# Optimization experiments

Measured on AMD Instinct MI355X. Metric: run time of the kernel, lower is better.

Reference implementation:

```python
import jax, jax.numpy as jnp
import numpy as np

B, L, D = 2, 2048, 2048
N, K, H = 16, 8, 128
EPS = 1e-6
ROPE_THETA = 1000000
K_MASK = -2.3819763e+38


def rms_norm(x, w, eps=EPS):
    dtype = x.dtype
    rms = jnp.sqrt(jnp.mean(x.astype(jnp.float32) ** 2, axis=-1, keepdims=True) + eps)
    return (w * x / rms).astype(dtype)


def apply_rope(inputs, positions, head_dim, rope_theta=ROPE_THETA):
    # inputs: [B, L, n, H], positions: [B, L]
    fraction = 2 * jnp.arange(0, head_dim // 2, dtype=jnp.float32) / head_dim
    timescale = rope_theta ** fraction  # [H/2]
    sinusoid = positions[..., jnp.newaxis] / timescale[jnp.newaxis, jnp.newaxis, :]  # [B,L,H/2]
    sinusoid = sinusoid[..., jnp.newaxis, :]  # [B,L,1,H/2]
    sin, cos = jnp.sin(sinusoid), jnp.cos(sinusoid)
    first, second = jnp.split(inputs, 2, axis=-1)
    out = jnp.concatenate([first * cos - second * sin, second * cos + first * sin], axis=-1)
    return out.astype(inputs.dtype)


def setup_inputs() -> dict:
    key = jax.random.key(0)
    ks = jax.random.split(key, 6)
    x = jax.random.normal(ks[0], (B, L, D), dtype=jnp.float32)
    position_ids = jnp.broadcast_to(jnp.arange(L, dtype=jnp.int32)[None, :], (B, L))
    # causal mask [B, L, S]
    attn_mask = jnp.broadcast_to(jnp.tril(jnp.ones((L, L), dtype=bool))[None], (B, L, L))
    wq = jax.random.normal(ks[1], (D, N, H), dtype=jnp.float32) * 0.02
    wk = jax.random.normal(ks[2], (D, K, H), dtype=jnp.float32) * 0.02
    wv = jax.random.normal(ks[3], (D, K, H), dtype=jnp.float32) * 0.02
    wo = jax.random.normal(ks[4], (N, H, D), dtype=jnp.float32) * 0.02
    q_norm_w = jnp.ones((H,), dtype=jnp.float32)
    k_norm_w = jnp.ones((H,), dtype=jnp.float32)
    return {"x": x, "position_ids": position_ids, "attn_mask": attn_mask,
            "wq": wq, "wk": wk, "wv": wv, "wo": wo,
            "q_norm_w": q_norm_w, "k_norm_w": k_norm_w}


def reference(x, position_ids, attn_mask, wq, wk, wv, wo, q_norm_w, k_norm_w):
    scale = H ** (-0.5)
    q = jnp.einsum('BLD,DNH->BLNH', x, wq)  # [B,L,N,H]
    k = jnp.einsum('BSD,DKH->BSKH', x, wk)  # [B,S,K,H]
    v = jnp.einsum('BSD,DKH->BSKH', x, wv)
    q = rms_norm(q, q_norm_w)
    k = rms_norm(k, k_norm_w)
    q = apply_rope(q, position_ids, H)
    k = apply_rope(k, position_ids, H)
    b, l, n, h = q.shape
    s = k.shape[1]
    kk = k.shape[2]
    q = q.reshape((b, l, kk, n // kk, h))
    attn = jnp.einsum('BLKGH,BSKH->BKGLS', q, k) * scale
    attn = attn.reshape((b, n, l, s))
    attn = jnp.where(jnp.expand_dims(attn_mask, -3), attn, K_MASK)
    attn = jax.nn.softmax(attn.astype(jnp.float32), axis=-1).astype(k.dtype)
    attn = attn.reshape((b, kk, n // kk, l, s))
    qkv = jnp.einsum('BKGLS,BSKH->BLKGH', attn, v).reshape((b, l, n, h))
    out = jnp.einsum('BLNH,NHD->BLD', qkv, wo)
    return out
```

## Files before the change

### kernel.cpp

```cpp
#include <hip/hip_runtime.h>

#define B_ 2
#define L_ 2048
#define D_ 2048
#define NH_ 16
#define KH_ 8
#define HD_ 128

typedef __attribute__((ext_vector_type(8))) short short8;
typedef __attribute__((ext_vector_type(4))) short short4v;
typedef __attribute__((ext_vector_type(4))) float floatx4;

__device__ __forceinline__ unsigned short f2bf(float f) {
  unsigned u = __float_as_uint(f);
  unsigned r = (u + 0x7fffu + ((u >> 16) & 1u)) >> 16;
  return (unsigned short)r;
}
__device__ __forceinline__ float bf2f(unsigned short h) {
  return __uint_as_float(((unsigned)h) << 16);
}
__device__ __forceinline__ void gl_lds16(const void* g, void* l) {
  __builtin_amdgcn_global_load_lds(
      (const __attribute__((address_space(1))) unsigned int*)g,
      (__attribute__((address_space(3))) unsigned int*)l, 16, 0, 0);
}
__device__ __forceinline__ void barrier_lds_only() {
  asm volatile("s_waitcnt lgkmcnt(0)" ::: "memory");
  __builtin_amdgcn_s_barrier();
}

__global__ __launch_bounds__(256) void prep1(const float* __restrict__ x,
                                             const float* __restrict__ wq,
                                             const float* __restrict__ wk,
                                             const float* __restrict__ wv,
                                             const float* __restrict__ wo,
                                             unsigned short* __restrict__ xb,
                                             unsigned short* __restrict__ wqkv_t,
                                             unsigned short* __restrict__ wo_t) {
  int id = blockIdx.x;
  int t = threadIdx.x;
  if (id < 8192) {
    long i = ((long)id * 256 + t) * 4;
    float4 v = *(const float4*)(x + i);
    ushort4 o;
    o.x = f2bf(v.x); o.y = f2bf(v.y); o.z = f2bf(v.z); o.w = f2bf(v.w);
    *(ushort4*)(xb + i) = o;
    return;
  }
  id -= 8192;
  __shared__ float tile[32][33];
  const float* in;
  unsigned short* out;
  int C, sh;
  if (id < 4096) {
    in = wq; out = wqkv_t; C = 2048; sh = 6;
  } else if (id < 6144) {
    in = wk; out = wqkv_t + 2048L * 2048; C = 1024; sh = 5; id -= 4096;
  } else if (id < 8192) {
    in = wv; out = wqkv_t + 3072L * 2048; C = 1024; sh = 5; id -= 6144;
  } else {
    in = wo; out = wo_t; C = 2048; sh = 6; id -= 8192;
  }
  int c0 = (id & ((1 << sh) - 1)) * 32, r0 = (id >> sh) * 32;
  int tx = t & 31, ty = t >> 5;
#pragma unroll
  for (int i = 0; i < 4; i++)
    tile[ty + i * 8][tx] = in[(long)(r0 + ty + i * 8) * C + c0 + tx];
  __syncthreads();
#pragma unroll
  for (int i = 0; i < 4; i++) {
    int oc = ty + i * 8;
    out[(long)(c0 + oc) * 2048 + r0 + tx] = f2bf(tile[tx][oc]);
  }
}

__global__ __launch_bounds__(256) void prep2(const unsigned short* __restrict__ qkv,
                                             const int* __restrict__ pos,
                                             const float* __restrict__ qw,
                                             const float* __restrict__ kw,
                                             unsigned short* __restrict__ qo,
                                             unsigned short* __restrict__ ko,
                                             unsigned short* __restrict__ vT) {
  int id = blockIdx.x;
  int t = threadIdx.x;
  if (id < 24576) {
    const int lane = t & 63, w = t >> 6;
    const int gid = id * 4 + w;
    const int row = gid / 24;
    const int hd = gid - row * 24;
    const int b = row >> 11, l = row & 2047;
    const unsigned short* src = qkv + (long)row * 4096 + hd * 128;
    float x0 = bf2f(src[lane]);
    float x1 = bf2f(src[lane + 64]);
    float ss = x0 * x0 + x1 * x1;
#pragma unroll
    for (int off = 32; off; off >>= 1) ss += __shfl_xor(ss, off);
    float inv = 1.0f / sqrtf(ss * (1.0f / 128.0f) + 1e-6f);
    const float* nw = (hd < 16) ? qw : kw;
    x0 = nw[lane] * x0 * inv;
    x1 = nw[lane + 64] * x1 * inv;
    float p = (float)pos[row];
    float ang = p * exp2f((float)lane * -0.31143075889f);
    float s, c;
    sincosf(ang, &s, &c);
    float o0 = x0 * c - x1 * s;
    float o1 = x1 * c + x0 * s;
    unsigned short* dst;
    if (hd < 16) {
      const float QSC = 0.08838834764831845f * 1.4426950408889634f;
      o0 *= QSC;
      o1 *= QSC;
      dst = qo + (((long)b * NH_ + hd) * L_ + l) * HD_;
    } else {
      dst = ko + (((long)b * KH_ + (hd - 16)) * L_ + l) * HD_;
    }
    dst[lane] = f2bf(o0);
    dst[lane + 64] = f2bf(o1);
    return;
  }
  id -= 24576;
  __shared__ unsigned short tile[32][33];
  int l0 = (id & 63) * 32, h0 = ((id >> 6) & 3) * 32;
  int bk = id >> 8;
  int b = bk >> 3, kh = bk & 7;
  int tx = t & 31, ty = t >> 5;
  const unsigned short* src = qkv + (long)b * L_ * 4096 + 3072 + kh * 128;
#pragma unroll
  for (int i = 0; i < 4; i++)
    tile[ty + i * 8][tx] = src[(long)(l0 + ty + i * 8) * 4096 + h0 + tx];
  __syncthreads();
  unsigned short* dst = vT + (long)bk * HD_ * L_;
#pragma unroll
  for (int i = 0; i < 4; i++)
    dst[(long)(h0 + ty + i * 8) * L_ + l0 + tx] = tile[tx][ty + i * 8];
}

template <int MODE>
__global__ __launch_bounds__(256, 3) void gemm128(const unsigned short* __restrict__ A,
                                                  const unsigned short* __restrict__ Bt,
                                                  void* __restrict__ C,
                                                  int M, int N, int K) {
  __shared__ unsigned short As[128 * 64];
  __shared__ unsigned short Bs[128 * 64];
  const int t = threadIdx.x;
  const int lane = t & 63, w = t >> 6;
  const int wy = w >> 1, wx = w & 1;
  const int col = lane & 15, quad = lane >> 4;
  const long m0 = (long)blockIdx.y * 128, n0 = (long)blockIdx.x * 128;
  floatx4 acc[4][4];
#pragma unroll
  for (int i = 0; i < 4; i++)
#pragma unroll
    for (int j = 0; j < 4; j++) acc[i][j] = (floatx4)0.0f;
  const int rs = t >> 3, bs = t & 7;
  for (int kt = 0; kt < K; kt += 64) {
#pragma unroll
    for (int i = 0; i < 4; i++) {
      int r = i * 32 + rs;
      gl_lds16(A + (m0 + r) * (long)K + kt + ((bs ^ (r & 7)) << 3),
               &As[(i * 32 + w * 8) * 64]);
      gl_lds16(Bt + (n0 + r) * (long)K + kt + ((bs ^ (r & 7)) << 3),
               &Bs[(i * 32 + w * 8) * 64]);
    }
    __syncthreads();
#pragma unroll
    for (int ks = 0; ks < 2; ks++) {
      short8 af[4], bf[4];
#pragma unroll
      for (int mi = 0; mi < 4; mi++) {
        int row = wy * 64 + mi * 16 + col;
        int blk = ks * 4 + quad;
        af[mi] = *(const short8*)&As[row * 64 + ((blk ^ (row & 7)) << 3)];
      }
#pragma unroll
      for (int ni = 0; ni < 4; ni++) {
        int row = wx * 64 + ni * 16 + col;
        int blk = ks * 4 + quad;
        bf[ni] = *(const short8*)&Bs[row * 64 + ((blk ^ (row & 7)) << 3)];
      }
#pragma unroll
      for (int mi = 0; mi < 4; mi++)
#pragma unroll
        for (int ni = 0; ni < 4; ni++)
          acc[mi][ni] = __builtin_amdgcn_mfma_f32_16x16x32_bf16(af[mi], bf[ni],
                                                                acc[mi][ni], 0, 0, 0);
    }
    __syncthreads();
  }
#pragma unroll
  for (int mi = 0; mi < 4; mi++)
#pragma unroll
    for (int r = 0; r < 4; r++) {
      long row = m0 + wy * 64 + mi * 16 + quad * 4 + r;
#pragma unroll
      for (int ni = 0; ni < 4; ni++) {
        long cg = n0 + wx * 64 + ni * 16 + col;
        float val = acc[mi][ni][r];
        if (MODE == 1)
          ((unsigned short*)C)[row * N + cg] = f2bf(val);
        else
          ((float*)C)[row * N + cg] = val;
      }
    }
}

template <int MODE>
__global__ __launch_bounds__(512, 2) void gemm256(const unsigned short* __restrict__ A,
                                                  const unsigned short* __restrict__ Bt,
                                                  void* __restrict__ C,
                                                  int M, int N, int K) {
  __shared__ unsigned short As[2][256 * 64];
  __shared__ unsigned short Bs[2][256 * 64];
  const int t = threadIdx.x;
  const int lane = t & 63, w = t >> 6;
  const int wy = w >> 2, wx = w & 3;
  const int col = lane & 15, quad = lane >> 4;
  const long m0 = (long)blockIdx.y * 256, n0 = (long)blockIdx.x * 256;
  const int rs = t >> 3, bs = t & 7;
  const int nt = K >> 6;

#define SA256(bufi, Tt, h)                                                      \
  gl_lds16(A + (m0 + (h) * 64 + rs) * (long)K + (long)(Tt) * 64 +               \
               ((bs ^ (rs & 7)) << 3),                                          \
           &As[bufi][((h) * 64 + w * 8) * 64])
#define SB256(bufi, Tt, h)                                                      \
  gl_lds16(Bt + (n0 + (h) * 64 + rs) * (long)K + (long)(Tt) * 64 +              \
                ((bs ^ (rs & 7)) << 3),                                         \
           &Bs[bufi][((h) * 64 + w * 8) * 64])

  floatx4 acc[8][4];
#pragma unroll
  for (int i = 0; i < 8; i++)
#pragma unroll
    for (int j = 0; j < 4; j++) acc[i][j] = (floatx4)0.0f;

  SA256(0, 0, 0); SA256(0, 0, 1); SA256(0, 0, 2); SA256(0, 0, 3);
  SB256(0, 0, 0); SB256(0, 0, 1); SB256(0, 0, 2); SB256(0, 0, 3);
  SB256(1, 1, 0); SB256(1, 1, 1); SB256(1, 1, 2); SB256(1, 1, 3);
  asm volatile("s_waitcnt vmcnt(4)" ::: "memory");
  __builtin_amdgcn_s_barrier();

  for (int T = 0; T < nt; ++T) {
    const int c = T & 1;
    const unsigned short* Ac = As[c];
    const unsigned short* Bc = Bs[c];
    short8 a[4][2], b[4][2];

#pragma unroll
    for (int mi = 0; mi < 4; mi++)
#pragma unroll
      for (int ks = 0; ks < 2; ks++) {
        int row = wy * 128 + mi * 16 + col;
        a[mi][ks] = *(const short8*)&Ac[row * 64 + (((ks * 4 + quad) ^ (row & 7)) << 3)];
      }
#pragma unroll
    for (int ni = 0; ni < 2; ni++)
#pragma unroll
      for (int ks = 0; ks < 2; ks++) {
        int row = wx * 64 + ni * 16 + col;
        b[ni][ks] = *(const short8*)&Bc[row * 64 + (((ks * 4 + quad) ^ (row & 7)) << 3)];
      }
    if (T + 1 < nt) { SA256(c ^ 1, T + 1, 0); SA256(c ^ 1, T + 1, 2); }
    __builtin_amdgcn_s_barrier();
    asm volatile("s_waitcnt lgkmcnt(0)" ::: "memory");
    __builtin_amdgcn_s_setprio(1);
#pragma unroll
    for (int mi = 0; mi < 4; mi++)
#pragma unroll
      for (int ni = 0; ni < 2; ni++)
#pragma unroll
        for (int ks = 0; ks < 2; ks++)
          acc[mi][ni] = __builtin_amdgcn_mfma_f32_16x16x32_bf16(a[mi][ks], b[ni][ks],
                                                                acc[mi][ni], 0, 0, 0);
    __builtin_amdgcn_s_setprio(0);
    __builtin_amdgcn_s_barrier();

#pragma unroll
    for (int ni = 2; ni < 4; ni++)
#pragma unroll
      for (int ks = 0; ks < 2; ks++) {
        int row = wx * 64 + ni * 16 + col;
        b[ni][ks] = *(const short8*)&Bc[row * 64 + (((ks * 4 + quad) ^ (row & 7)) << 3)];
      }
    if (T + 1 < nt) { SA256(c ^ 1, T + 1, 1); SA256(c ^ 1, T + 1, 3); }
    __builtin_amdgcn_s_barrier();
    asm volatile("s_waitcnt lgkmcnt(0)" ::: "memory");
    __builtin_amdgcn_s_setprio(1);
#pragma unroll
    for (int mi = 0; mi < 4; mi++)
#pragma unroll
      for (int ni = 2; ni < 4; ni++)
#pragma unroll
        for (int ks = 0; ks < 2; ks++)
          acc[mi][ni] = __builtin_amdgcn_mfma_f32_16x16x32_bf16(a[mi][ks], b[ni][ks],
                                                                acc[mi][ni], 0, 0, 0);
    __builtin_amdgcn_s_setprio(0);
    __builtin_amdgcn_s_barrier();

#pragma unroll
    for (int mi = 0; mi < 4; mi++)
#pragma unroll
      for (int ks = 0; ks < 2; ks++) {
        int row = wy * 128 + (mi + 4) * 16 + col;
        a[mi][ks] = *(const short8*)&Ac[row * 64 + (((ks * 4 + quad) ^ (row & 7)) << 3)];
      }
    if (T + 2 < nt) { SB256(c, T + 2, 0); SB256(c, T + 2, 1); }
    __builtin_amdgcn_s_barrier();
    asm volatile("s_waitcnt lgkmcnt(0)" ::: "memory");
    __builtin_amdgcn_s_setprio(1);
#pragma unroll
    for (int mi = 0; mi < 4; mi++)
#pragma unroll
      for (int ni = 0; ni < 2; ni++)
#pragma unroll
        for (int ks = 0; ks < 2; ks++)
          acc[mi + 4][ni] = __builtin_amdgcn_mfma_f32_16x16x32_bf16(a[mi][ks], b[ni][ks],
                                                                    acc[mi + 4][ni], 0, 0, 0);
    __builtin_amdgcn_s_setprio(0);
    __builtin_amdgcn_s_barrier();

    if (T + 2 < nt) { SB256(c, T + 2, 2); SB256(c, T + 2, 3); }
    __builtin_amdgcn_s_setprio(1);
#pragma unroll
    for (int mi = 0; mi < 4; mi++)
#pragma unroll
      for (int ni = 2; ni < 4; ni++)
#pragma unroll
        for (int ks = 0; ks < 2; ks++)
          acc[mi + 4][ni] = __builtin_amdgcn_mfma_f32_16x16x32_bf16(a[mi][ks], b[ni][ks],
                                                                    acc[mi + 4][ni], 0, 0, 0);
    __builtin_amdgcn_s_setprio(0);
    if (T + 1 < nt) {
      if (T >= nt - 2)
        asm volatile("s_waitcnt vmcnt(0)" ::: "memory");
      else
        asm volatile("s_waitcnt vmcnt(4)" ::: "memory");
      __builtin_amdgcn_s_barrier();
    }
  }
#undef SA256
#undef SB256

#pragma unroll
  for (int mi = 0; mi < 8; mi++)
#pragma unroll
    for (int r = 0; r < 4; r++) {
      long row = m0 + wy * 128 + mi * 16 + quad * 4 + r;
#pragma unroll
      for (int ni = 0; ni < 4; ni++) {
        long cg = n0 + wx * 64 + ni * 16 + col;
        float val = acc[mi][ni][r];
        if (MODE == 1)
          ((unsigned short*)C)[row * N + cg] = f2bf(val);
        else
          ((float*)C)[row * N + cg] = val;
      }
    }
}

__global__ __launch_bounds__(256, 2) void flash(const unsigned short* __restrict__ Q,
                                                const unsigned short* __restrict__ Kg,
                                                const unsigned short* __restrict__ VT,
                                                unsigned short* __restrict__ Og,
                                                float* __restrict__ Opart,
                                                float* __restrict__ lpart) {
  __shared__ unsigned short Ks[64 * 128];
  __shared__ unsigned short Vs[128 * 64];
  __shared__ unsigned short Ps[128 * 72];
  const int id = blockIdx.x;
  const int g = id & 255, r3 = id >> 8;
  const int kk3 = g & 7, nb = g >> 3;
  const int n = nb & 15, b = nb >> 4;
  int qt, st0, st1, chunk;
  if (r3 == 0) {
    qt = kk3; chunk = -1; st0 = 0; st1 = 2 * qt + 2;
  } else {
    qt = 15 - kk3;
    chunk = r3 - 1;
    const int half = qt + 1;
    st0 = chunk ? half : 0;
    st1 = chunk ? 2 * half : half;
  }
  const int steps_full = 2 * qt + 2;
  const int t = threadIdx.x, lane = t & 63, w = t >> 6;
  const int col = lane & 15, quad = lane >> 4;
  const int kvh = n >> 1;
  const unsigned short* kb = Kg + ((long)b * KH_ + kvh) * L_ * HD_;
  const unsigned short* vtb = VT + ((long)b * KH_ + kvh) * HD_ * L_;
  const int l0 = qt * 128;
  const unsigned short* qb = Q + (((long)b * NH_ + n) * L_ + l0) * HD_;

  const int rK = t >> 4, blkK = t & 15;
  const int rV = t >> 3, blkV = t & 7;

  short8 qf[2][4];
#pragma unroll
  for (int mi = 0; mi < 2; mi++)
#pragma unroll
    for (int ks = 0; ks < 4; ks++)
      qf[mi][ks] = *(const short8*)(qb + (w * 32 + mi * 16 + col) * 128 + ks * 32 + quad * 8);

  floatx4 o[2][8];
#pragma unroll
  for (int mi = 0; mi < 2; mi++)
#pragma unroll
    for (int nf = 0; nf < 8; nf++) o[mi][nf] = (floatx4)0.0f;
  float lrow[2] = {0.0f, 0.0f};

  {
    const long sb = (long)st0 * 64;
#pragma unroll
    for (int i = 0; i < 4; i++) {
      int r = i * 16 + rK;
      int gblk = (blkK & 8) | ((blkK ^ r) & 7);
      gl_lds16(kb + (sb + r) * 128 + gblk * 8, &Ks[(i * 16 + w * 4) * 128]);
    }
#pragma unroll
    for (int j = 0; j < 4; j++) {
      int r = j * 32 + rV;
      int gblk = (blkV ^ r) & 7;
      gl_lds16(vtb + (long)r * L_ + sb + gblk * 8, &Vs[(j * 32 + w * 8) * 64]);
    }
  }
  __syncthreads();

  short8 kpre[4], vpre[4];
  if (st0 + 1 < st1) {
    const long s0n = (long)(st0 + 1) * 64;
#pragma unroll
    for (int i = 0; i < 4; i++) {
      int r = i * 16 + rK;
      int gblk = (blkK & 8) | ((blkK ^ r) & 7);
      kpre[i] = *(const short8*)(kb + (s0n + r) * 128 + gblk * 8);
    }
#pragma unroll
    for (int j = 0; j < 4; j++) {
      int r = j * 32 + rV;
      int gblk = (blkV ^ r) & 7;
      vpre[j] = *(const short8*)(vtb + (long)r * L_ + s0n + gblk * 8);
    }
  }

  for (int st = st0; st < st1; st++) {
    const int s0 = st * 64;

    floatx4 sa[2][4];
#pragma unroll
    for (int mi = 0; mi < 2; mi++)
#pragma unroll
      for (int sf = 0; sf < 4; sf++) sa[mi][sf] = (floatx4)0.0f;
#pragma unroll
    for (int ks = 0; ks < 4; ks++) {
      short8 bf[4];
#pragma unroll
      for (int sf = 0; sf < 4; sf++) {
        int srow = sf * 16 + col;
        int blk = ks * 4 + quad;
        bf[sf] = *(const short8*)&Ks[srow * 128 + (((blk & 8) | ((blk ^ srow) & 7)) << 3)];
      }
#pragma unroll
      for (int mi = 0; mi < 2; mi++)
#pragma unroll
        for (int sf = 0; sf < 4; sf++)
          sa[mi][sf] = __builtin_amdgcn_mfma_f32_16x16x32_bf16(bf[sf], qf[mi][ks],
                                                               sa[mi][sf], 0, 0, 0);
    }

    if (st >= steps_full - 2) {
#pragma unroll
      for (int mi = 0; mi < 2; mi++) {
        int lg = l0 + w * 32 + mi * 16 + col;
#pragma unroll
        for (int sf = 0; sf < 4; sf++)
#pragma unroll
          for (int r = 0; r < 4; r++) {
            int sg = s0 + sf * 16 + quad * 4 + r;
            if (sg > lg) sa[mi][sf][r] = -3.0e38f;
          }
      }
    }

#pragma unroll
    for (int mi = 0; mi < 2; mi++)
#pragma unroll
      for (int sf = 0; sf < 4; sf++) {
        short4v pk;
#pragma unroll
        for (int r = 0; r < 4; r++) {
          float pv = exp2f(sa[mi][sf][r] - 17.0f);
          lrow[mi] += pv;
          pk[r] = (short)f2bf(pv);
        }
        *(short4v*)&Ps[(w * 32 + mi * 16 + col) * 72 + sf * 16 + quad * 4] = pk;
      }

#pragma unroll
    for (int ks = 0; ks < 2; ks++) {
      short8 pf[2];
#pragma unroll
      for (int mi = 0; mi < 2; mi++)
        pf[mi] = *(const short8*)&Ps[(w * 32 + mi * 16 + col) * 72 + ks * 32 + quad * 8];
      short8 vf[8];
#pragma unroll
      for (int nf = 0; nf < 8; nf++) {
        int h = nf * 16 + col;
        int blk = ks * 4 + quad;
        vf[nf] = *(const short8*)&Vs[h * 64 + ((blk ^ (h & 7)) << 3)];
      }
#pragma unroll
      for (int mi = 0; mi < 2; mi++)
#pragma unroll
        for (int nf = 0; nf < 8; nf++)
          o[mi][nf] = __builtin_amdgcn_mfma_f32_16x16x32_bf16(pf[mi], vf[nf],
                                                              o[mi][nf], 0, 0, 0);
    }

    barrier_lds_only();
    if (st + 1 < st1) {
#pragma unroll
      for (int i = 0; i < 4; i++) {
        int r = i * 16 + rK;
        *(short8*)&Ks[r * 128 + blkK * 8] = kpre[i];
      }
#pragma unroll
      for (int j = 0; j < 4; j++) {
        int r = j * 32 + rV;
        *(short8*)&Vs[r * 64 + blkV * 8] = vpre[j];
      }
      barrier_lds_only();
      if (st + 2 < st1) {
        const long s0n = (long)(st + 2) * 64;
#pragma unroll
        for (int i = 0; i < 4; i++) {
          int r = i * 16 + rK;
          int gblk = (blkK & 8) | ((blkK ^ r) & 7);
          kpre[i] = *(const short8*)(kb + (s0n + r) * 128 + gblk * 8);
        }
#pragma unroll
        for (int j = 0; j < 4; j++) {
          int r = j * 32 + rV;
          int gblk = (blkV ^ r) & 7;
          vpre[j] = *(const short8*)(vtb + (long)r * L_ + s0n + gblk * 8);
        }
      }
    }
  }

  if (chunk < 0) {
#pragma unroll
    for (int mi = 0; mi < 2; mi++) {
      float s = lrow[mi];
      s += __shfl_xor(s, 16);
      s += __shfl_xor(s, 32);
#pragma unroll
      for (int r = 0; r < 4; r++) {
        float inv = 1.0f / __shfl(s, quad * 4 + r);
        int lg = l0 + w * 32 + mi * 16 + quad * 4 + r;
        unsigned short* dst = Og + (((long)b * L_ + lg) * NH_ + n) * HD_;
#pragma unroll
        for (int nf = 0; nf < 8; nf++)
          dst[nf * 16 + col] = f2bf(o[mi][nf][r] * inv);
      }
    }
  } else {
    const int pidx = (((b * NH_ + n) * 8) + (qt - 8)) * 2 + chunk;
    float* Od = Opart + (long)pidx * 16384;
#pragma unroll
    for (int mi = 0; mi < 2; mi++) {
      float s = lrow[mi];
      s += __shfl_xor(s, 16);
      s += __shfl_xor(s, 32);
      if (lane < 16) lpart[pidx * 128 + w * 32 + mi * 16 + lane] = s;
#pragma unroll
      for (int r = 0; r < 4; r++) {
        int rl = w * 32 + mi * 16 + quad * 4 + r;
#pragma unroll
        for (int nf = 0; nf < 8; nf++)
          Od[rl * 128 + nf * 16 + col] = o[mi][nf][r];
      }
    }
  }
}

__global__ __launch_bounds__(256) void combine(const float* __restrict__ Opart,
                                               const float* __restrict__ lpart,
                                               unsigned short* __restrict__ Og) {
  const int id = blockIdx.x;
  const int q8 = id & 7, n = (id >> 3) & 15, b = id >> 7;
  const int pidx = (((b * NH_ + n) * 8) + q8) * 2;
  const float* OA = Opart + (long)pidx * 16384;
  const float* OB = OA + 16384;
  const int t = threadIdx.x;
  const int r = t >> 1, c0 = (t & 1) * 64;
  const float inv = 1.0f / (lpart[pidx * 128 + r] + lpart[(pidx + 1) * 128 + r]);
  const int lg = (8 + q8) * 128 + r;
  unsigned short* dst = Og + (((long)b * L_ + lg) * NH_ + n) * HD_ + c0;
#pragma unroll
  for (int c = 0; c < 64; c += 4) {
    float4 a = *(const float4*)(OA + r * 128 + c0 + c);
    float4 bb = *(const float4*)(OB + r * 128 + c0 + c);
    ushort4 ov;
    ov.x = f2bf((a.x + bb.x) * inv);
    ov.y = f2bf((a.y + bb.y) * inv);
    ov.z = f2bf((a.z + bb.z) * inv);
    ov.w = f2bf((a.w + bb.w) * inv);
    *(ushort4*)(dst + c) = ov;
  }
}

extern "C" void kernel_launch(void* const* d_in, const int* in_sizes, int n_in,
                              void* d_out, int out_size, void* d_ws, size_t ws_size,
                              hipStream_t stream) {
  const float* x = (const float*)d_in[0];
  const int* pos = (const int*)d_in[1];
  const float* wq = (const float*)d_in[3];
  const float* wk = (const float*)d_in[4];
  const float* wv = (const float*)d_in[5];
  const float* wo = (const float*)d_in[6];
  const float* qnw = (const float*)d_in[7];
  const float* knw = (const float*)d_in[8];
  float* out = (float*)d_out;

  char* ws = (char*)d_ws;
  unsigned short* xb     = (unsigned short*)(ws + 0);
  unsigned short* wqkv_t = (unsigned short*)(ws + 16777216);
  unsigned short* wo_t   = (unsigned short*)(ws + 33554432);
  unsigned short* qkv    = (unsigned short*)(ws + 41943040);
  unsigned short* q      = (unsigned short*)(ws + 75497472);
  unsigned short* k      = (unsigned short*)(ws + 92274688);
  unsigned short* vT     = (unsigned short*)(ws + 100663296);
  unsigned short* ao     = (unsigned short*)(ws + 109051904);
  if (ws_size < 125829120) return;

  float* Opart = (float*)qkv;
  float* lpart = (float*)xb;

  prep1<<<20480, 256, 0, stream>>>(x, wq, wk, wv, wo, xb, wqkv_t, wo_t);
  gemm256<1><<<dim3(16, 16), 512, 0, stream>>>(xb, wqkv_t, qkv, 4096, 4096, 2048);
  prep2<<<28672, 256, 0, stream>>>(qkv, pos, qnw, knw, q, k, vT);
  flash<<<768, 256, 0, stream>>>(q, k, vT, ao, Opart, lpart);
  combine<<<256, 256, 0, stream>>>(Opart, lpart, ao);
  gemm128<0><<<dim3(16, 32), 256, 0, stream>>>(ao, wo_t, out, 4096, 2048, 2048);
}
```

Baseline: 353.6 us.

## Reorder GEMM global-to-LDS prefetch schedule with finer vmcnt waits

Reorganizes the double-buffered GEMM's global_load_lds prefetch schedule. Half of the next A tile is now issued two iterations ahead alongside the B halves, and the initial prologue interleaves A and B loads. Partial s_waitcnt vmcnt waits are added before each sub-phase, so each phase waits only for the loads it needs rather than draining at the end of the iteration. This aims to keep more loads in flight and hide memory latency, but the hand-counted vmcnt values must exactly match the issue order or the kernel will read stale LDS data.

```diff
diff --git a/kernel.cpp b/kernel.cpp
--- a/kernel.cpp
+++ b/kernel.cpp
@@ -234,10 +234,18 @@
 #pragma unroll
     for (int j = 0; j < 4; j++) acc[i][j] = (floatx4)0.0f;
 
-  SA256(0, 0, 0); SA256(0, 0, 1); SA256(0, 0, 2); SA256(0, 0, 3);
-  SB256(0, 0, 0); SB256(0, 0, 1); SB256(0, 0, 2); SB256(0, 0, 3);
-  SB256(1, 1, 0); SB256(1, 1, 1); SB256(1, 1, 2); SB256(1, 1, 3);
-  asm volatile("s_waitcnt vmcnt(4)" ::: "memory");
+  SB256(0, 0, 0); SB256(0, 0, 1);
+  SA256(0, 0, 0); SA256(0, 0, 2);
+  SB256(0, 0, 2); SB256(0, 0, 3);
+  SA256(0, 0, 1); SA256(0, 0, 3);
+  if (nt > 1) {
+    SB256(1, 1, 0); SB256(1, 1, 1);
+    SA256(1, 1, 0); SA256(1, 1, 2);
+    SB256(1, 1, 2); SB256(1, 1, 3);
+    asm volatile("s_waitcnt vmcnt(10)" ::: "memory");
+  } else {
+    asm volatile("s_waitcnt vmcnt(0)" ::: "memory");
+  }
   __builtin_amdgcn_s_barrier();
 
   for (int T = 0; T < nt; ++T) {
@@ -260,7 +268,7 @@
         int row = wx * 64 + ni * 16 + col;
         b[ni][ks] = *(const short8*)&Bc[row * 64 + (((ks * 4 + quad) ^ (row & 7)) << 3)];
       }
-    if (T + 1 < nt) { SA256(c ^ 1, T + 1, 0); SA256(c ^ 1, T + 1, 2); }
+    if (T + 1 < nt) { SA256(c ^ 1, T + 1, 1); SA256(c ^ 1, T + 1, 3); }
     __builtin_amdgcn_s_barrier();
     asm volatile("s_waitcnt lgkmcnt(0)" ::: "memory");
     __builtin_amdgcn_s_setprio(1);
@@ -275,6 +283,10 @@
     __builtin_amdgcn_s_setprio(0);
     __builtin_amdgcn_s_barrier();
 
+    if (T < nt - 1)
+      asm volatile("s_waitcnt vmcnt(10)" ::: "memory");
+    else
+      asm volatile("s_waitcnt vmcnt(2)" ::: "memory");
 #pragma unroll
     for (int ni = 2; ni < 4; ni++)
 #pragma unroll
@@ -282,7 +294,6 @@
         int row = wx * 64 + ni * 16 + col;
         b[ni][ks] = *(const short8*)&Bc[row * 64 + (((ks * 4 + quad) ^ (row & 7)) << 3)];
       }
-    if (T + 1 < nt) { SA256(c ^ 1, T + 1, 1); SA256(c ^ 1, T + 1, 3); }
     __builtin_amdgcn_s_barrier();
     asm volatile("s_waitcnt lgkmcnt(0)" ::: "memory");
     __builtin_amdgcn_s_setprio(1);
@@ -297,6 +308,10 @@
     __builtin_amdgcn_s_setprio(0);
     __builtin_amdgcn_s_barrier();
 
+    if (T < nt - 1)
+      asm volatile("s_waitcnt vmcnt(8)" ::: "memory");
+    else
+      asm volatile("s_waitcnt vmcnt(0)" ::: "memory");
 #pragma unroll
     for (int mi = 0; mi < 4; mi++)
 #pragma unroll
@@ -319,7 +334,10 @@
     __builtin_amdgcn_s_setprio(0);
     __builtin_amdgcn_s_barrier();
 
-    if (T + 2 < nt) { SB256(c, T + 2, 2); SB256(c, T + 2, 3); }
+    if (T + 2 < nt) {
+      SA256(c, T + 2, 0); SA256(c, T + 2, 2);
+      SB256(c, T + 2, 2); SB256(c, T + 2, 3);
+    }
     __builtin_amdgcn_s_setprio(1);
 #pragma unroll
     for (int mi = 0; mi < 4; mi++)
@@ -331,8 +349,8 @@
                                                                     acc[mi + 4][ni], 0, 0, 0);
     __builtin_amdgcn_s_setprio(0);
     if (T + 1 < nt) {
-      if (T >= nt - 2)
-        asm volatile("s_waitcnt vmcnt(0)" ::: "memory");
+      if (T <= nt - 3)
+        asm volatile("s_waitcnt vmcnt(10)" ::: "memory");
       else
         asm volatile("s_waitcnt vmcnt(4)" ::: "memory");
       __builtin_amdgcn_s_barrier();
```

New measurement: 351.3 us. Within noise of the previous version (-0.6%).
